# Kernel tuning notes

Hardware: AMD Instinct MI355X
Metric: run time of the kernel (lower is better)

## Reference

```python
import jax, jax.numpy as jnp
import numpy as np

B, N_PIC, C, H, W, P = 32, 4, 3, 224, 224, 16
HP = H // P  # 14
NP = HP * HP  # 196 patches
D = C * P * P  # 768 = hidden_size


def setup_inputs() -> dict:
    key = jax.random.key(0)
    ks = jax.random.split(key, 12)
    s = 0.02
    def lin(k, din, dout):
        kw, kb = jax.random.split(k)
        return (jax.random.normal(kw, (din, dout), jnp.float32) * s,
                jax.random.normal(kb, (dout,), jnp.float32) * s)
    W1, b1 = lin(ks[0], D, D)
    Wq, bq = lin(ks[1], D, D)
    Wk, bk = lin(ks[2], D, D)
    Wv, bv = lin(ks[3], D, D)
    Wo1, bo1 = lin(ks[4], D, D)
    Wo2, bo2 = lin(ks[5], D, D)
    x = jax.random.normal(ks[6], (B, N_PIC, C, H, W), jnp.float32)
    return {"x": x, "W1": W1, "b1": b1, "Wq": Wq, "bq": bq, "Wk": Wk,
            "bk": bk, "Wv": Wv, "bv": bv, "Wo1": Wo1, "bo1": bo1,
            "Wo2": Wo2, "bo2": bo2}


def reference(x, W1, b1, Wq, bq, Wk, bk, Wv, bv, Wo1, bo1, Wo2, bo2):
    b = x.shape[0]
    # patchify: matches torch unfold(3,P,P).unfold(4,P,P) + permute + view
    # -> [b, N, num_patches, C*P*P] with (C, ph, pw) ordering in last dim
    p = x.reshape(b, N_PIC, C, HP, P, HP, P)
    p = p.transpose(0, 1, 3, 5, 2, 4, 6).reshape(b, N_PIC, NP, D)
    h = p @ W1 + b1  # [b, N, S, D]
    # attention: query always from picture 0; key/value per picture (batched)
    Q = h[:, 0] @ Wq + bq          # [b, S, D]
    K = h @ Wk + bk                # [b, N, S, D]
    V = h @ Wv + bv                # [b, N, S, D]
    scale = 1.0 / jnp.sqrt(jnp.float32(D))
    scores = jnp.einsum('bsd,bnmd->bnsm', Q, K) * scale  # [b, N, S, S]
    attn = jax.nn.softmax(scores, axis=-1)
    wv = jnp.einsum('bnsm,bnmd->bnsd', attn, V)           # [b, N, S, D]
    out = jax.nn.relu(wv @ Wo1 + bo1) @ Wo2 + bo2
    return out
```

## Files before the change

kernel.cpp:

```cpp
#include <hip/hip_runtime.h>

typedef __bf16 bf16;
typedef __bf16 bf16x8 __attribute__((ext_vector_type(8)));
typedef float  f32x4  __attribute__((ext_vector_type(4)));


__global__ __launch_bounds__(256) void patchify_k(const float* __restrict__ x,
                                                  bf16* __restrict__ p) {
  int t = blockIdx.x * 256 + threadIdx.x;
  if (t >= 128 * 3 * 14 * 16 * 14) return;
  int j  = t % 14; t /= 14;
  int ph = t % 16; t /= 16;
  int i  = t % 14; t /= 14;
  int c  = t % 3;  t /= 3;
  int bn = t;
  const float* src = x + (((long long)(bn * 3 + c) * 224 + (i * 16 + ph)) * 224 + j * 16);
  bf16* dst = p + ((long long)(bn * 196 + (i * 14 + j)) * 768 + c * 256 + ph * 16);
  bf16 tmp[16];
  for (int k = 0; k < 16; k += 4) {
    float4 f = *(const float4*)(src + k);
    tmp[k + 0] = (bf16)f.x; tmp[k + 1] = (bf16)f.y;
    tmp[k + 2] = (bf16)f.z; tmp[k + 3] = (bf16)f.w;
  }
  *(bf16x8*)(dst)     = *(bf16x8*)&tmp[0];
  *(bf16x8*)(dst + 8) = *(bf16x8*)&tmp[8];
}

__global__ __launch_bounds__(256) void wtrans_k(const float* __restrict__ w0,
                                                const float* __restrict__ w1,
                                                const float* __restrict__ w2,
                                                const float* __restrict__ w3,
                                                const float* __restrict__ w4,
                                                const float* __restrict__ w5,
                                                bf16* __restrict__ out) {
  __shared__ float tile[32][33];
  const float* W;
  switch (blockIdx.z) {
    case 0: W = w0; break; case 1: W = w1; break; case 2: W = w2; break;
    case 3: W = w3; break; case 4: W = w4; break; default: W = w5; break;
  }
  bf16* o = out + (long long)blockIdx.z * 768 * 768;
  int nb = blockIdx.x * 32, kb = blockIdx.y * 32;
  int c = threadIdx.x & 31, r = threadIdx.x >> 5;
  for (int rr = 0; rr < 32; rr += 8)
    tile[r + rr][c] = W[(long long)(kb + r + rr) * 768 + nb + c];
  __syncthreads();
  for (int rr = 0; rr < 32; rr += 8)
    o[(long long)(nb + r + rr) * 768 + kb + c] = (bf16)tile[c][r + rr];
}

__global__ __launch_bounds__(256) void vtrans_k(const bf16* __restrict__ kv,
                                                bf16* __restrict__ Vt) {
  __shared__ short tile[32][33];
  int z = blockIdx.z;
  const short* v = (const short*)(kv + (long long)z * 301056 + 768);
  short* vt = (short*)(Vt + (long long)z * 768 * 224);
  int db = blockIdx.x * 32;
  int mb = blockIdx.y * 32;
  int c = threadIdx.x & 31, r = threadIdx.x >> 5;
  for (int rr = 0; rr < 32; rr += 8) {
    int m = mb + r + rr;
    short val = 0;
    if (m < 196) val = v[(long long)m * 1536 + db + c];
    tile[r + rr][c] = val;
  }
  __syncthreads();
  for (int rr = 0; rr < 32; rr += 8) {
    int d = db + r + rr;
    vt[(long long)d * 224 + mb + c] = tile[c][r + rr];
  }
}

__global__ __launch_bounds__(64) void softmax_k(const float* __restrict__ S,
                                                bf16* __restrict__ attn) {
  const int row = blockIdx.x;
  const float* sr = S + (long long)row * 196;
  const int l = threadIdx.x;
  float v0 = sr[l];
  float v1 = sr[l + 64];
  float v2 = sr[l + 128];
  float v3 = (l + 192 < 196) ? sr[l + 192] : -1e30f;
  float mx = fmaxf(fmaxf(v0, v1), fmaxf(v2, v3));
  for (int o = 32; o > 0; o >>= 1) mx = fmaxf(mx, __shfl_xor(mx, o));
  float e0 = __expf(v0 - mx);
  float e1 = __expf(v1 - mx);
  float e2 = __expf(v2 - mx);
  float e3 = (l + 192 < 196) ? __expf(v3 - mx) : 0.f;
  float s = e0 + e1 + e2 + e3;
  for (int o = 32; o > 0; o >>= 1) s += __shfl_xor(s, o);
  float inv = 1.0f / s;
  bf16* ar = attn + (long long)row * 224;
  ar[l]       = (bf16)(e0 * inv);
  ar[l + 64]  = (bf16)(e1 * inv);
  ar[l + 128] = (bf16)(e2 * inv);
  int m3 = l + 192;
  if (m3 < 196) ar[m3] = (bf16)(e3 * inv);
  else if (m3 < 224) ar[m3] = (bf16)0.0f;
}

__device__ __forceinline__ void gld16(const bf16* g, bf16* l) {
  __builtin_amdgcn_global_load_lds(
      (const __attribute__((address_space(1))) unsigned int*)g,
      (__attribute__((address_space(3))) unsigned int*)l, 16, 0, 0);
}

__global__ __launch_bounds__(256) void gemm128(
    const bf16* __restrict__ A, const bf16* __restrict__ Bt,
    const float* __restrict__ bias, const float* __restrict__ bias2,
    void* __restrict__ Cout,
    int M, int N, int K, int lda, int ldb, int gr, long long gs,
    long long strideAz, int a_zdiv, long long strideBz, long long strideCz,
    float scale, int relu, int out_bf16) {
  __shared__ __align__(16) char smem[34816];
  bf16* AsBuf = (bf16*)smem;
  bf16* BsBuf = (bf16*)(smem + 16384);

  const int tid = threadIdx.x;
  const int lane = tid & 63;
  const int w = tid >> 6;
  const int wm = w & 1, wn = w >> 1;
  const int z = blockIdx.z;
  const int n0 = blockIdx.x * 128, m0 = blockIdx.y * 128;

  const bf16* Az  = A  + (long long)(z / a_zdiv) * strideAz;
  const bf16* Btz = Bt + (long long)z * strideBz;

  const int rl  = 16 * w + (lane & 15);
  const int kc8 = (lane >> 4) * 8;
  int ar0 = m0 + rl;        if (ar0 >= M) ar0 = M - 1;
  int ar1 = m0 + 64 + rl;   if (ar1 >= M) ar1 = M - 1;
  const bf16* aP0 = Az + (long long)(ar0 / gr) * gs + (long long)(ar0 % gr) * lda + kc8;
  const bf16* aP1 = Az + (long long)(ar1 / gr) * gs + (long long)(ar1 % gr) * lda + kc8;
  int br0 = n0 + rl;        if (br0 >= N) br0 = N - 1;
  int br1 = n0 + 64 + rl;   if (br1 >= N) br1 = N - 1;
  const bf16* bP0 = Btz + (long long)br0 * ldb + kc8;
  const bf16* bP1 = Btz + (long long)br1 * ldb + kc8;

  const int dstOff = w * 512;

#define ISSUE(t, buf) do { const int _o = (t) << 5;                 \
    gld16(aP0 + _o, AsBuf + (buf) * 4096 + dstOff);                 \
    gld16(aP1 + _o, AsBuf + (buf) * 4096 + 2048 + dstOff);          \
    gld16(bP0 + _o, BsBuf + (buf) * 4096 + dstOff);                 \
    gld16(bP1 + _o, BsBuf + (buf) * 4096 + 2048 + dstOff); } while (0)

  const int niter = K >> 5;
  f32x4 acc[4][4] = {};
  const int fr = lane & 15, fq = lane >> 4;

  ISSUE(0, 0);

  for (int i = 0; i < niter; ++i) {
    __syncthreads();
    const int cur = i & 1;
    if (i + 1 < niter) ISSUE(i + 1, cur ^ 1);

    const bf16* Ac = AsBuf + cur * 4096;
    const bf16* Bc = BsBuf + cur * 4096;
    bf16x8 a[4], b[4];
#pragma unroll
    for (int mi = 0; mi < 4; mi++)
      a[mi] = *(const bf16x8*)&Ac[(wm * 4 + mi) * 512 + fq * 128 + fr * 8];
#pragma unroll
    for (int ni = 0; ni < 4; ni++)
      b[ni] = *(const bf16x8*)&Bc[(wn * 4 + ni) * 512 + fq * 128 + fr * 8];
#pragma unroll
    for (int mi = 0; mi < 4; mi++)
#pragma unroll
      for (int ni = 0; ni < 4; ni++)
        acc[mi][ni] = __builtin_amdgcn_mfma_f32_16x16x32_bf16(a[mi], b[ni], acc[mi][ni], 0, 0, 0);
  }
#undef ISSUE

  __syncthreads();

  const long long cz = (long long)z * strideCz;
  if (out_bf16) {
    bf16* Cs = (bf16*)smem;
#pragma unroll
    for (int ni = 0; ni < 4; ni++) {
      int col = wn * 64 + ni * 16 + fr;
      int gcol = n0 + col;
      float bb = 0.f;
      if (bias) bb = (bias2 && gcol >= 768) ? bias2[gcol - 768] : bias[gcol];
#pragma unroll
      for (int mi = 0; mi < 4; mi++) {
        int rbase = wm * 64 + mi * 16 + fq * 4;
#pragma unroll
        for (int r = 0; r < 4; r++) {
          float v = acc[mi][ni][r] * scale + bb;
          if (relu) v = fmaxf(v, 0.f);
          Cs[(rbase + r) * 136 + col] = (bf16)v;
        }
      }
    }
    __syncthreads();
    bf16* Cp = (bf16*)Cout;
    const int rr = tid >> 4, cc = (tid & 15) * 8;
#pragma unroll
    for (int pp = 0; pp < 8; pp++) {
      int row = pp * 16 + rr;
      int grow = m0 + row;
      if (grow < M)
        *(bf16x8*)(Cp + cz + (long long)grow * N + n0 + cc) =
            *(const bf16x8*)&Cs[row * 136 + cc];
    }
  } else {
    float* Cs = (float*)smem;
    float* Cp = (float*)Cout;
    for (int half = 0; half < 2; ++half) {
      if (wm == half) {
#pragma unroll
        for (int ni = 0; ni < 4; ni++) {
          int col = wn * 64 + ni * 16 + fr;
          int gcol = n0 + col;
          float bb = 0.f;
          if (bias && gcol < N)
            bb = (bias2 && gcol >= 768) ? bias2[gcol - 768] : bias[gcol];
#pragma unroll
          for (int mi = 0; mi < 4; mi++) {
            int rbase = mi * 16 + fq * 4;
#pragma unroll
            for (int r = 0; r < 4; r++) {
              float v = acc[mi][ni][r] * scale + bb;
              if (relu) v = fmaxf(v, 0.f);
              Cs[(rbase + r) * 132 + col] = v;
            }
          }
        }
      }
      __syncthreads();
      const int rr = tid >> 5, cc = (tid & 31) * 4;
#pragma unroll
      for (int pp = 0; pp < 8; pp++) {
        int row = pp * 8 + rr;
        int grow = m0 + half * 64 + row;
        if (grow < M) {
          int gcol = n0 + cc;
          float* dst = Cp + cz + (long long)grow * N + gcol;
          const float* srcl = &Cs[row * 132 + cc];
          if (gcol + 4 <= N) {
            *(float4*)dst = *(const float4*)srcl;
          } else {
            for (int e = 0; e < 4; e++)
              if (gcol + e < N) dst[e] = srcl[e];
          }
        }
      }
      __syncthreads();
    }
  }
}

extern "C" void kernel_launch(void* const* d_in, const int* in_sizes, int n_in,
                              void* d_out, int out_size, void* d_ws, size_t ws_size,
                              hipStream_t stream) {
  (void)in_sizes; (void)n_in; (void)out_size; (void)ws_size;
  const float* x   = (const float*)d_in[0];
  const float* W1  = (const float*)d_in[1];
  const float* b1  = (const float*)d_in[2];
  const float* Wq  = (const float*)d_in[3];
  const float* bq  = (const float*)d_in[4];
  const float* Wk  = (const float*)d_in[5];
  const float* bk  = (const float*)d_in[6];
  const float* Wv  = (const float*)d_in[7];
  const float* bv  = (const float*)d_in[8];
  const float* Wo1 = (const float*)d_in[9];
  const float* bo1 = (const float*)d_in[10];
  const float* Wo2 = (const float*)d_in[11];
  const float* bo2 = (const float*)d_in[12];

  char* ws = (char*)d_ws;
  bf16*  p    = (bf16*)(ws + 0);
  bf16*  vt   = (bf16*)(ws + 0);
  bf16*  h    = (bf16*)(ws + 44040192LL);
  bf16*  wv   = (bf16*)(ws + 44040192LL);
  bf16*  kv   = (bf16*)(ws + 82575360LL);
  bf16*  o1   = (bf16*)(ws + 82575360LL);
  float* sc   = (float*)(ws + 159645696LL);
  bf16*  q    = (bf16*)(ws + 179314688LL);
  bf16*  attn = (bf16*)(ws + 179314688LL);
  bf16*  wt   = (bf16*)(ws + 190554112LL);
  constexpr long long WSZ = 768LL * 768;

  const float qk_scale = 0.03608439182435161f;

  patchify_k<<<4704, 256, 0, stream>>>(x, p);
  wtrans_k<<<dim3(24, 24, 6), 256, 0, stream>>>(W1, Wk, Wv, Wq, Wo1, Wo2, wt);

  gemm128<<<dim3(6, 196, 1), 256, 0, stream>>>(p, wt + 0 * WSZ, b1, nullptr, h,
      25088, 768, 768, 768, 768, 25088, 0LL, 0LL, 1, 0LL, 0LL, 1.f, 0, 1);
  gemm128<<<dim3(12, 196, 1), 256, 0, stream>>>(h, wt + 1 * WSZ, bk, bv, kv,
      25088, 1536, 768, 768, 768, 25088, 0LL, 0LL, 1, 0LL, 0LL, 1.f, 0, 1);
  gemm128<<<dim3(6, 49, 1), 256, 0, stream>>>(h, wt + 3 * WSZ, bq, nullptr, q,
      6272, 768, 768, 768, 768, 196, 602112LL, 0LL, 1, 0LL, 0LL, 1.f, 0, 1);
  vtrans_k<<<dim3(24, 7, 128), 256, 0, stream>>>(kv, vt);
  gemm128<<<dim3(2, 2, 128), 256, 0, stream>>>(q, kv, nullptr, nullptr, sc,
      196, 196, 768, 768, 1536, 196, 0LL, 150528LL, 4, 301056LL, 38416LL,
      qk_scale, 0, 0);
  softmax_k<<<25088, 64, 0, stream>>>(sc, attn);
  gemm128<<<dim3(6, 2, 128), 256, 0, stream>>>(attn, vt, nullptr, nullptr, wv,
      196, 768, 224, 224, 224, 196, 0LL, 43904LL, 1, 172032LL, 150528LL,
      1.f, 0, 1);
  gemm128<<<dim3(6, 196, 1), 256, 0, stream>>>(wv, wt + 4 * WSZ, bo1, nullptr, o1,
      25088, 768, 768, 768, 768, 25088, 0LL, 0LL, 1, 0LL, 0LL, 1.f, 1, 1);
  gemm128<<<dim3(6, 196, 1), 256, 0, stream>>>(o1, wt + 5 * WSZ, bo2, nullptr,
      (float*)d_out,
      25088, 768, 768, 768, 768, 25088, 0LL, 0LL, 1, 0LL, 0LL, 1.f, 0, 0);
}
```

Measured before the change: 601.5 us.

## Add 256x256-tile pipelined GEMM for the large dense projections

Adds a new 512-thread GEMM kernel with 256x256 output tiles, double-buffered direct-to-LDS global loads interleaved with MFMA phases, swizzled LDS layout, priority hints, and XCD-aware block remapping. It replaces the 128-tile GEMM for the four large M=25088 projections (W1, K/V, Wo1, Wo2). The aim is more data reuse per tile and better overlap of loads with matrix ops. The cost is higher register and LDS use, and a kernel that assumes M, N and K are multiples of its tile sizes.

```diff
diff --git a/kernel.cpp b/kernel.cpp
--- a/kernel.cpp
+++ b/kernel.cpp
@@ -252,6 +252,217 @@
   }
 }
 
+__global__ __launch_bounds__(512, 2) void gemm256(
+    const bf16* __restrict__ A, const bf16* __restrict__ Bt,
+    const float* __restrict__ bias, const float* __restrict__ bias2,
+    void* __restrict__ Cout,
+    int N, int K, int lda, int ldb, int relu, int out_bf16) {
+  __shared__ __align__(16) char smem[131072];
+  bf16* As = (bf16*)smem;
+  bf16* Bs = (bf16*)(smem + 65536);
+
+  const int tid = threadIdx.x;
+  const int lane = tid & 63;
+  const int w = tid >> 6;
+  const int wm = w >> 2;
+  const int wn = w & 3;
+
+  const int nx = N >> 8;
+  const int nwg = gridDim.x * gridDim.y;
+  int f = blockIdx.y * gridDim.x + blockIdx.x;
+  {
+    const int q = nwg >> 3, r = nwg & 7;
+    const int xcd = f & 7, idx = f >> 3;
+    f = (xcd < r ? xcd * (q + 1) : r * (q + 1) + (xcd - r) * q) + idx;
+  }
+  const int n0 = (f % nx) * 256;
+  const int m0 = (f / nx) * 256;
+
+  const int srow = ((tid >> 2) & 15) + ((tid >> 7) << 4);
+  const int scol = ((tid >> 6) & 1) * 32 +
+                   (((tid & 3) << 3) ^ ((tid & 32) ? 16 : 0));
+  const bf16* aBase = A  + (long long)(m0 + srow) * lda + scol;
+  const bf16* bBase = Bt + (long long)(n0 + srow) * ldb + scol;
+  const int ldsw = w * 512;
+
+#define STG(base, ld, dstArr, buf, kt, hh) do {                              \
+    const bf16* _s = (base) + (long long)((hh) * 128) * (ld) + (kt) * 64;    \
+    gld16(_s,               (dstArr) + (buf) * 16384 + (hh) * 8192 + ldsw);  \
+    gld16(_s + 64LL * (ld), (dstArr) + (buf) * 16384 + (hh) * 8192 + 4096 + ldsw); \
+  } while (0)
+
+  const int fr = lane & 15, fq = lane >> 4;
+  const int frij = fr * 32 + ((fq * 8) ^ ((fr & 8) ? 16 : 0));
+  const bf16* aRd = As + wm * 8192 + frij;
+  const bf16* bRd = Bs + (wn >> 1) * 8192 + (wn & 1) * 4096 + frij;
+
+  f32x4 acc[8][4] = {};
+  bf16x8 aF[4][2], bF[4][2];
+
+  const int nt = K >> 6;
+
+  STG(aBase, lda, As, 0, 0, 0);
+  STG(aBase, lda, As, 0, 0, 1);
+  STG(bBase, ldb, Bs, 0, 0, 0);
+  STG(bBase, ldb, Bs, 0, 0, 1);
+  STG(bBase, ldb, Bs, 1, 1, 0);
+  STG(aBase, lda, As, 1, 1, 0);
+  asm volatile("s_waitcnt vmcnt(4)" ::: "memory");
+  asm volatile("s_barrier" ::: "memory");
+
+  for (int t = 0; t < nt; ++t) {
+    const int buf = t & 1;
+    const int bOff = buf << 14;
+
+#pragma unroll
+    for (int mi = 0; mi < 4; ++mi)
+#pragma unroll
+      for (int kk = 0; kk < 2; ++kk)
+        aF[mi][kk] = *(const bf16x8*)(aRd + bOff + mi * 1024 + kk * 512);
+#pragma unroll
+    for (int ni = 0; ni < 2; ++ni)
+#pragma unroll
+      for (int kk = 0; kk < 2; ++kk)
+        bF[ni][kk] = *(const bf16x8*)(bRd + bOff + ni * 1024 + kk * 512);
+    if (t + 1 < nt) STG(aBase, lda, As, buf ^ 1, t + 1, 1);
+    asm volatile("s_barrier" ::: "memory");
+    __builtin_amdgcn_s_setprio(1);
+#pragma unroll
+    for (int mi = 0; mi < 4; ++mi)
+#pragma unroll
+      for (int ni = 0; ni < 2; ++ni)
+#pragma unroll
+        for (int kk = 0; kk < 2; ++kk)
+          acc[mi][ni] = __builtin_amdgcn_mfma_f32_16x16x32_bf16(
+              aF[mi][kk], bF[ni][kk], acc[mi][ni], 0, 0, 0);
+    __builtin_amdgcn_s_setprio(0);
+    asm volatile("s_barrier" ::: "memory");
+
+#pragma unroll
+    for (int ni = 2; ni < 4; ++ni)
+#pragma unroll
+      for (int kk = 0; kk < 2; ++kk)
+        bF[ni][kk] = *(const bf16x8*)(bRd + bOff + ni * 1024 + kk * 512);
+    if (t + 1 < nt) STG(bBase, ldb, Bs, buf ^ 1, t + 1, 1);
+    asm volatile("s_barrier" ::: "memory");
+    __builtin_amdgcn_s_setprio(1);
+#pragma unroll
+    for (int mi = 0; mi < 4; ++mi)
+#pragma unroll
+      for (int ni = 2; ni < 4; ++ni)
+#pragma unroll
+        for (int kk = 0; kk < 2; ++kk)
+          acc[mi][ni] = __builtin_amdgcn_mfma_f32_16x16x32_bf16(
+              aF[mi][kk], bF[ni][kk], acc[mi][ni], 0, 0, 0);
+    __builtin_amdgcn_s_setprio(0);
+    asm volatile("s_barrier" ::: "memory");
+
+#pragma unroll
+    for (int mi = 0; mi < 4; ++mi)
+#pragma unroll
+      for (int kk = 0; kk < 2; ++kk)
+        aF[mi][kk] = *(const bf16x8*)(aRd + bOff + (4 + mi) * 1024 + kk * 512);
+    if (t + 2 < nt) STG(bBase, ldb, Bs, buf, t + 2, 0);
+    asm volatile("s_barrier" ::: "memory");
+    __builtin_amdgcn_s_setprio(1);
+#pragma unroll
+    for (int mi = 0; mi < 4; ++mi)
+#pragma unroll
+      for (int ni = 0; ni < 2; ++ni)
+#pragma unroll
+        for (int kk = 0; kk < 2; ++kk)
+          acc[4 + mi][ni] = __builtin_amdgcn_mfma_f32_16x16x32_bf16(
+              aF[mi][kk], bF[ni][kk], acc[4 + mi][ni], 0, 0, 0);
+    __builtin_amdgcn_s_setprio(0);
+    asm volatile("s_barrier" ::: "memory");
+
+    if (t + 2 < nt) STG(aBase, lda, As, buf, t + 2, 0);
+    asm volatile("s_barrier" ::: "memory");
+    __builtin_amdgcn_s_setprio(1);
+#pragma unroll
+    for (int mi = 0; mi < 4; ++mi)
+#pragma unroll
+      for (int ni = 2; ni < 4; ++ni)
+#pragma unroll
+        for (int kk = 0; kk < 2; ++kk)
+          acc[4 + mi][ni] = __builtin_amdgcn_mfma_f32_16x16x32_bf16(
+              aF[mi][kk], bF[ni][kk], acc[4 + mi][ni], 0, 0, 0);
+    __builtin_amdgcn_s_setprio(0);
+    if (t < nt - 2)       asm volatile("s_waitcnt vmcnt(4)" ::: "memory");
+    else if (t == nt - 2) asm volatile("s_waitcnt vmcnt(0)" ::: "memory");
+    asm volatile("s_barrier" ::: "memory");
+  }
+#undef STG
+
+  const long long Nll = N;
+  if (out_bf16) {
+    bf16* Cs = (bf16*)smem;
+    bf16* Cp = (bf16*)Cout;
+#pragma unroll
+    for (int half = 0; half < 2; ++half) {
+      if (wm == half) {
+#pragma unroll
+        for (int ni = 0; ni < 4; ++ni) {
+          const int col = wn * 64 + ni * 16 + fr;
+          const int gcol = n0 + col;
+          float bb = 0.f;
+          if (bias) bb = (bias2 && gcol >= 768) ? bias2[gcol - 768] : bias[gcol];
+#pragma unroll
+          for (int mi = 0; mi < 8; ++mi) {
+#pragma unroll
+            for (int r = 0; r < 4; ++r) {
+              float v = acc[mi][ni][r] + bb;
+              if (relu) v = fmaxf(v, 0.f);
+              Cs[(mi * 16 + fq * 4 + r) * 268 + col] = (bf16)v;
+            }
+          }
+        }
+      }
+      __syncthreads();
+      const int row = tid >> 2, cb = (tid & 3) * 8;
+      const bf16* srcl = &Cs[row * 268 + cb];
+      bf16* dst = Cp + (long long)(m0 + half * 128 + row) * Nll + n0 + cb;
+#pragma unroll
+      for (int j = 0; j < 8; ++j)
+        *(bf16x8*)(dst + j * 32) = *(const bf16x8*)(srcl + j * 32);
+      __syncthreads();
+    }
+  } else {
+    float* Cs = (float*)smem;
+    float* Cp = (float*)Cout;
+#pragma unroll
+    for (int pass = 0; pass < 4; ++pass) {
+      if (wm == (pass >> 1)) {
+#pragma unroll
+        for (int ni = 0; ni < 4; ++ni) {
+          const int col = wn * 64 + ni * 16 + fr;
+          const int gcol = n0 + col;
+          float bb = 0.f;
+          if (bias) bb = (bias2 && gcol >= 768) ? bias2[gcol - 768] : bias[gcol];
+#pragma unroll
+          for (int mi2 = 0; mi2 < 4; ++mi2) {
+            const int mi = (pass & 1) * 4 + mi2;
+#pragma unroll
+            for (int r = 0; r < 4; ++r) {
+              float v = acc[mi][ni][r] + bb;
+              if (relu) v = fmaxf(v, 0.f);
+              Cs[(mi2 * 16 + fq * 4 + r) * 268 + col] = v;
+            }
+          }
+        }
+      }
+      __syncthreads();
+      const int row = tid >> 3, c4 = (tid & 7) * 4;
+      const float* srcl = &Cs[row * 268 + c4];
+      float* dst = Cp + (long long)(m0 + pass * 64 + row) * Nll + n0 + c4;
+#pragma unroll
+      for (int j = 0; j < 8; ++j)
+        *(float4*)(dst + j * 32) = *(const float4*)(srcl + j * 32);
+      __syncthreads();
+    }
+  }
+}
+
 extern "C" void kernel_launch(void* const* d_in, const int* in_sizes, int n_in,
                               void* d_out, int out_size, void* d_ws, size_t ws_size,
                               hipStream_t stream) {
@@ -288,10 +499,10 @@
   patchify_k<<<4704, 256, 0, stream>>>(x, p);
   wtrans_k<<<dim3(24, 24, 6), 256, 0, stream>>>(W1, Wk, Wv, Wq, Wo1, Wo2, wt);
 
-  gemm128<<<dim3(6, 196, 1), 256, 0, stream>>>(p, wt + 0 * WSZ, b1, nullptr, h,
-      25088, 768, 768, 768, 768, 25088, 0LL, 0LL, 1, 0LL, 0LL, 1.f, 0, 1);
-  gemm128<<<dim3(12, 196, 1), 256, 0, stream>>>(h, wt + 1 * WSZ, bk, bv, kv,
-      25088, 1536, 768, 768, 768, 25088, 0LL, 0LL, 1, 0LL, 0LL, 1.f, 0, 1);
+  gemm256<<<dim3(3, 98), 512, 0, stream>>>(p, wt + 0 * WSZ, b1, nullptr, h,
+      768, 768, 768, 768, 0, 1);
+  gemm256<<<dim3(6, 98), 512, 0, stream>>>(h, wt + 1 * WSZ, bk, bv, kv,
+      1536, 768, 768, 768, 0, 1);
   gemm128<<<dim3(6, 49, 1), 256, 0, stream>>>(h, wt + 3 * WSZ, bq, nullptr, q,
       6272, 768, 768, 768, 768, 196, 602112LL, 0LL, 1, 0LL, 0LL, 1.f, 0, 1);
   vtrans_k<<<dim3(24, 7, 128), 256, 0, stream>>>(kv, vt);
@@ -302,9 +513,8 @@
   gemm128<<<dim3(6, 2, 128), 256, 0, stream>>>(attn, vt, nullptr, nullptr, wv,
       196, 768, 224, 224, 224, 196, 0LL, 43904LL, 1, 172032LL, 150528LL,
       1.f, 0, 1);
-  gemm128<<<dim3(6, 196, 1), 256, 0, stream>>>(wv, wt + 4 * WSZ, bo1, nullptr, o1,
-      25088, 768, 768, 768, 768, 25088, 0LL, 0LL, 1, 0LL, 0LL, 1.f, 1, 1);
-  gemm128<<<dim3(6, 196, 1), 256, 0, stream>>>(o1, wt + 5 * WSZ, bo2, nullptr,
-      (float*)d_out,
-      25088, 768, 768, 768, 768, 25088, 0LL, 0LL, 1, 0LL, 0LL, 1.f, 0, 0);
-}
+  gemm256<<<dim3(3, 98), 512, 0, stream>>>(wv, wt + 4 * WSZ, bo1, nullptr, o1,
+      768, 768, 768, 768, 1, 1);
+  gemm256<<<dim3(3, 98), 512, 0, stream>>>(o1, wt + 5 * WSZ, bo2, nullptr,
+      (float*)d_out, 768, 768, 768, 768, 0, 0);
+}
```

Result: faster. 557.6 us (-7.3%).

## Add 128x256-tile GEMM for large projections and pack four softmax rows per block

Applied to the files above, without the earlier changes.

Adds a specialised GEMM kernel with 128x256 output tiles, double-buffered 16-byte global-to-LDS loads, XCD-aware block remapping and an LDS-staged epilogue. It is used for the four large 25088-row projections (W1, K/V, Wo1, Wo2) in place of the generic 128x128 GEMM. The larger tile raises operand reuse and halves the number of workgroups, but needs more accumulator registers per thread and may lower occupancy. Softmax now handles four rows per 256-thread block instead of one row per 64-thread block, to cut block launch and scheduling overhead.

```diff
diff --git a/kernel.cpp b/kernel.cpp
--- a/kernel.cpp
+++ b/kernel.cpp
@@ -71,11 +71,11 @@
   }
 }
 
-__global__ __launch_bounds__(64) void softmax_k(const float* __restrict__ S,
-                                                bf16* __restrict__ attn) {
-  const int row = blockIdx.x;
+__global__ __launch_bounds__(256) void softmax_k(const float* __restrict__ S,
+                                                 bf16* __restrict__ attn) {
+  const int row = blockIdx.x * 4 + (threadIdx.x >> 6);
   const float* sr = S + (long long)row * 196;
-  const int l = threadIdx.x;
+  const int l = threadIdx.x & 63;
   float v0 = sr[l];
   float v1 = sr[l + 64];
   float v2 = sr[l + 128];
@@ -252,6 +252,140 @@
   }
 }
 
+__global__ __launch_bounds__(256, 2) void gemm_bn256(
+    const bf16* __restrict__ A, const bf16* __restrict__ Bt,
+    const float* __restrict__ bias, const float* __restrict__ bias2,
+    void* __restrict__ Cout,
+    int N, int K, int lda, int ldb, int relu, int out_bf16) {
+  __shared__ __align__(16) char smem[49152];
+  bf16* As = (bf16*)smem;
+  bf16* Bs = (bf16*)(smem + 16384);
+
+  const int tid = threadIdx.x;
+  const int lane = tid & 63;
+  const int w = tid >> 6;
+
+  const int nx = N >> 8;
+  const int nwg = gridDim.x * gridDim.y;
+  int f = blockIdx.y * gridDim.x + blockIdx.x;
+  {
+    const int q = nwg >> 3, r = nwg & 7;
+    const int xcd = f & 7, idx = f >> 3;
+    f = (xcd < r ? xcd * (q + 1) : r * (q + 1) + (xcd - r) * q) + idx;
+  }
+  const int n0 = (f % nx) * 256;
+  const int m0 = (f / nx) * 128;
+
+  const int rl  = 16 * w + (lane & 15);
+  const int kc8 = (lane >> 4) * 8;
+  const bf16* aSrc = A  + (long long)(m0 + rl) * lda + kc8;
+  const bf16* bSrc = Bt + (long long)(n0 + rl) * ldb + kc8;
+  const int dstOff = w * 512;
+
+#define ISSUE(t, buf) do { const long long _o = (long long)(t) << 5;           \
+    gld16(aSrc + _o,                  As + (buf) * 4096 + dstOff);             \
+    gld16(aSrc + 64LL * lda + _o,     As + (buf) * 4096 + 2048 + dstOff);      \
+    gld16(bSrc + _o,                  Bs + (buf) * 8192 + dstOff);             \
+    gld16(bSrc + 64LL * ldb + _o,     Bs + (buf) * 8192 + 2048 + dstOff);      \
+    gld16(bSrc + 128LL * ldb + _o,    Bs + (buf) * 8192 + 4096 + dstOff);      \
+    gld16(bSrc + 192LL * ldb + _o,    Bs + (buf) * 8192 + 6144 + dstOff); } while (0)
+
+  const int niter = K >> 5;
+  f32x4 acc[8][4] = {};
+  const int fr = lane & 15, fq = lane >> 4;
+
+  ISSUE(0, 0);
+
+  for (int i = 0; i < niter; ++i) {
+    __syncthreads();
+    const int cur = i & 1;
+    if (i + 1 < niter) ISSUE(i + 1, cur ^ 1);
+
+    const bf16* Ac = As + cur * 4096;
+    const bf16* Bc = Bs + cur * 8192 + w * 2048;
+    bf16x8 a[8], b[4];
+#pragma unroll
+    for (int mi = 0; mi < 8; mi++)
+      a[mi] = *(const bf16x8*)&Ac[mi * 512 + fq * 128 + fr * 8];
+#pragma unroll
+    for (int ni = 0; ni < 4; ni++)
+      b[ni] = *(const bf16x8*)&Bc[ni * 512 + fq * 128 + fr * 8];
+#pragma unroll
+    for (int mi = 0; mi < 8; mi++)
+#pragma unroll
+      for (int ni = 0; ni < 4; ni++)
+        acc[mi][ni] = __builtin_amdgcn_mfma_f32_16x16x32_bf16(a[mi], b[ni], acc[mi][ni], 0, 0, 0);
+  }
+#undef ISSUE
+
+  __syncthreads();
+
+  const long long Nll = N;
+  if (out_bf16) {
+    bf16* Cs = (bf16*)smem;
+    bf16* Cp = (bf16*)Cout;
+#pragma unroll
+    for (int half = 0; half < 2; ++half) {
+#pragma unroll
+      for (int ni = 0; ni < 4; ++ni) {
+        const int col = w * 64 + ni * 16 + fr;
+        const int gcol = n0 + col;
+        float bb = 0.f;
+        if (bias) bb = (bias2 && gcol >= 768) ? bias2[gcol - 768] : bias[gcol];
+#pragma unroll
+        for (int mi2 = 0; mi2 < 4; ++mi2) {
+          const int mi = half * 4 + mi2;
+#pragma unroll
+          for (int r = 0; r < 4; ++r) {
+            float v = acc[mi][ni][r] + bb;
+            if (relu) v = fmaxf(v, 0.f);
+            Cs[(mi2 * 16 + fq * 4 + r) * 264 + col] = (bf16)v;
+          }
+        }
+      }
+      __syncthreads();
+      const int row = tid >> 2, cb = (tid & 3) * 8;
+      const bf16* srcl = &Cs[row * 264 + cb];
+      bf16* dst = Cp + (long long)(m0 + half * 64 + row) * Nll + n0 + cb;
+#pragma unroll
+      for (int j = 0; j < 8; ++j)
+        *(bf16x8*)(dst + j * 32) = *(const bf16x8*)(srcl + j * 32);
+      __syncthreads();
+    }
+  } else {
+    float* Cs = (float*)smem;
+    float* Cp = (float*)Cout;
+#pragma unroll
+    for (int pass = 0; pass < 4; ++pass) {
+#pragma unroll
+      for (int ni = 0; ni < 4; ++ni) {
+        const int col = w * 64 + ni * 16 + fr;
+        const int gcol = n0 + col;
+        float bb = 0.f;
+        if (bias) bb = (bias2 && gcol >= 768) ? bias2[gcol - 768] : bias[gcol];
+#pragma unroll
+        for (int mi2 = 0; mi2 < 2; ++mi2) {
+          const int mi = pass * 2 + mi2;
+#pragma unroll
+          for (int r = 0; r < 4; ++r) {
+            float v = acc[mi][ni][r] + bb;
+            if (relu) v = fmaxf(v, 0.f);
+            Cs[(mi2 * 16 + fq * 4 + r) * 264 + col] = v;
+          }
+        }
+      }
+      __syncthreads();
+      const int row = tid >> 3, c4 = (tid & 7) * 4;
+      const float* srcl = &Cs[row * 264 + c4];
+      float* dst = Cp + (long long)(m0 + pass * 32 + row) * Nll + n0 + c4;
+#pragma unroll
+      for (int j = 0; j < 8; ++j)
+        *(float4*)(dst + j * 32) = *(const float4*)(srcl + j * 32);
+      __syncthreads();
+    }
+  }
+}
+
 extern "C" void kernel_launch(void* const* d_in, const int* in_sizes, int n_in,
                               void* d_out, int out_size, void* d_ws, size_t ws_size,
                               hipStream_t stream) {
@@ -288,23 +422,22 @@
   patchify_k<<<4704, 256, 0, stream>>>(x, p);
   wtrans_k<<<dim3(24, 24, 6), 256, 0, stream>>>(W1, Wk, Wv, Wq, Wo1, Wo2, wt);
 
-  gemm128<<<dim3(6, 196, 1), 256, 0, stream>>>(p, wt + 0 * WSZ, b1, nullptr, h,
-      25088, 768, 768, 768, 768, 25088, 0LL, 0LL, 1, 0LL, 0LL, 1.f, 0, 1);
-  gemm128<<<dim3(12, 196, 1), 256, 0, stream>>>(h, wt + 1 * WSZ, bk, bv, kv,
-      25088, 1536, 768, 768, 768, 25088, 0LL, 0LL, 1, 0LL, 0LL, 1.f, 0, 1);
+  gemm_bn256<<<dim3(3, 196), 256, 0, stream>>>(p, wt + 0 * WSZ, b1, nullptr, h,
+      768, 768, 768, 768, 0, 1);
+  gemm_bn256<<<dim3(6, 196), 256, 0, stream>>>(h, wt + 1 * WSZ, bk, bv, kv,
+      1536, 768, 768, 768, 0, 1);
   gemm128<<<dim3(6, 49, 1), 256, 0, stream>>>(h, wt + 3 * WSZ, bq, nullptr, q,
       6272, 768, 768, 768, 768, 196, 602112LL, 0LL, 1, 0LL, 0LL, 1.f, 0, 1);
   vtrans_k<<<dim3(24, 7, 128), 256, 0, stream>>>(kv, vt);
   gemm128<<<dim3(2, 2, 128), 256, 0, stream>>>(q, kv, nullptr, nullptr, sc,
       196, 196, 768, 768, 1536, 196, 0LL, 150528LL, 4, 301056LL, 38416LL,
       qk_scale, 0, 0);
-  softmax_k<<<25088, 64, 0, stream>>>(sc, attn);
+  softmax_k<<<6272, 256, 0, stream>>>(sc, attn);
   gemm128<<<dim3(6, 2, 128), 256, 0, stream>>>(attn, vt, nullptr, nullptr, wv,
       196, 768, 224, 224, 224, 196, 0LL, 43904LL, 1, 172032LL, 150528LL,
       1.f, 0, 1);
-  gemm128<<<dim3(6, 196, 1), 256, 0, stream>>>(wv, wt + 4 * WSZ, bo1, nullptr, o1,
-      25088, 768, 768, 768, 768, 25088, 0LL, 0LL, 1, 0LL, 0LL, 1.f, 1, 1);
-  gemm128<<<dim3(6, 196, 1), 256, 0, stream>>>(o1, wt + 5 * WSZ, bo2, nullptr,
-      (float*)d_out,
-      25088, 768, 768, 768, 768, 25088, 0LL, 0LL, 1, 0LL, 0LL, 1.f, 0, 0);
-}
+  gemm_bn256<<<dim3(3, 196), 256, 0, stream>>>(wv, wt + 4 * WSZ, bo1, nullptr, o1,
+      768, 768, 768, 768, 1, 1);
+  gemm_bn256<<<dim3(3, 196), 256, 0, stream>>>(o1, wt + 5 * WSZ, bo2, nullptr,
+      (float*)d_out, 768, 768, 768, 768, 0, 0);
+}
```

New measurement: 586.9 us. -2.4%, faster.
